# Kernel tuning notes

Hardware: AMD Instinct MI355X
Metric: run time of the kernel (lower is better)

Reference implementation:

```python
import jax, jax.numpy as jnp
import numpy as np

ALPHA, GAMMA = 0.25, 2.0
CLASS_W, COORD_W, MASK_W = 2.0, 5.0, 5.0
EPS = 1e-8


def point_sample(masks, coords):
    """Bilinear sample (grid_sample, align_corners=False, zero padding).
    masks: [R, H, W]; coords: [P, 2] as (x, y) in [0, 1]. Returns [R, P]."""
    H, W = masks.shape[-2:]
    gx = 2.0 * coords[:, 0] - 1.0
    gy = 2.0 * coords[:, 1] - 1.0
    x = ((gx + 1.0) * W - 1.0) * 0.5
    y = ((gy + 1.0) * H - 1.0) * 0.5
    x0 = jnp.floor(x)
    y0 = jnp.floor(y)
    wx1 = x - x0
    wy1 = y - y0
    wx0 = 1.0 - wx1
    wy0 = 1.0 - wy1
    x0i = x0.astype(jnp.int32)
    y0i = y0.astype(jnp.int32)
    x1i = x0i + 1
    y1i = y0i + 1

    def gather(ix, iy):
        valid = ((ix >= 0) & (ix < W) & (iy >= 0) & (iy < H)).astype(masks.dtype)
        ixc = jnp.clip(ix, 0, W - 1)
        iyc = jnp.clip(iy, 0, H - 1)
        return masks[:, iyc, ixc] * valid  # [R, P]

    return (gather(x0i, y0i) * (wx0 * wy0)
            + gather(x1i, y0i) * (wx1 * wy0)
            + gather(x0i, y1i) * (wx0 * wy1)
            + gather(x1i, y1i) * (wx1 * wy1))


def setup_inputs() -> dict:
    key = jax.random.key(0)
    k1, k2, k3, k4, k5, k6 = jax.random.split(key, 6)
    bs, Q, n_ctrl, Hm, Wm, T, P = 8, 300, 16, 128, 128, 160, 12544
    return {
        "pred_logits": jax.random.normal(k1, (bs, Q, 1), jnp.float32),
        "pred_ctrl_points": jax.random.uniform(k2, (bs, Q, n_ctrl, 2), jnp.float32),
        "pred_seg_mask": jax.random.normal(k3, (bs, Q, Hm, Wm), jnp.float32),
        "tgt_pts": jax.random.uniform(k4, (T, n_ctrl, 2), jnp.float32),
        "tgt_masks": jax.random.uniform(k5, (T, Hm, Wm), jnp.float32),
        "point_coords": jax.random.uniform(k6, (P, 2), jnp.float32),
        "lvl": 0,
    }


def reference(pred_logits, pred_ctrl_points, pred_seg_mask, tgt_pts, tgt_masks, point_coords, lvl):
    bs, Q = pred_logits.shape[:2]
    out_prob = jax.nn.sigmoid(pred_logits.reshape(bs * Q, -1))          # [N, 1]
    out_pts = pred_ctrl_points.reshape(bs * Q, -1)                      # [N, 2*n_ctrl]
    tgt_flat = tgt_pts.reshape(tgt_pts.shape[0], -1)                    # [T, 2*n_ctrl]

    cost_mask_dice = 0.0
    if lvl < 2:  # num_seg_layers
        out_masks = pred_seg_mask.reshape(bs * Q, *pred_seg_mask.shape[-2:])
        # nearest-interp of tgt_masks to out_masks size is identity (same size)
        t_pts_samp = point_sample(tgt_masks, point_coords)              # [T, P]
        o_pts_samp = point_sample(out_masks, point_coords)              # [N, P]
        s = jax.nn.sigmoid(o_pts_samp)                                  # dice_loss sigmoids inputs
        numerator = 2.0 * jnp.einsum('np,tp->nt', s, t_pts_samp)        # [N, T]
        denominator = s.sum(-1)[:, None] + t_pts_samp.sum(-1)[None, :]
        cost_mask_dice = 1.0 - (numerator + 1.0) / (denominator + 1.0)

    neg_cost = (1.0 - ALPHA) * out_prob ** GAMMA * (-jnp.log(1.0 - out_prob + EPS))
    pos_cost = ALPHA * (1.0 - out_prob) ** GAMMA * (-jnp.log(out_prob + EPS))
    cost_class = pos_cost - neg_cost                                    # [N, 1]

    cost_kpts = jnp.abs(out_pts[:, None, :] - tgt_flat[None, :, :]).sum(-1)  # L1 cdist [N, T]

    C = CLASS_W * cost_class + COORD_W * cost_kpts + MASK_W * cost_mask_dice
    return C.reshape(bs, Q, -1)
```

## Files before the change

### kernel.cpp

```cpp
#include <hip/hip_runtime.h>
#include <hip/hip_bf16.h>
#include <cstdint>

#define HW 128
#define MASK_ELEMS (HW * HW)
#define SBLK 1024
#define NBLK 256

typedef unsigned short ushort_t;
typedef __attribute__((ext_vector_type(4))) unsigned short ushort4_t;
typedef __attribute__((ext_vector_type(8))) short short8;
typedef __attribute__((ext_vector_type(4))) float f32x4;

__device__ __forceinline__ float asf(unsigned int u) {
    union { unsigned int i; float f; } c;
    c.i = u;
    return c.f;
}
__device__ __forceinline__ ushort_t f2bf(float f) {
    union { float f; unsigned int i; } c;
    c.f = f;
    unsigned int r = c.i + 0x7FFFu + ((c.i >> 16) & 1u);
    return (ushort_t)(r >> 16);
}

__global__ void kprep(const float* __restrict__ coords, int* __restrict__ idx,
                      uint2* __restrict__ wpk, int P) {
    int i = blockIdx.x * 256 + threadIdx.x;
    if (i >= P) return;
    float cx = coords[2 * i], cy = coords[2 * i + 1];
    float x = cx * (float)HW - 0.5f;
    float y = cy * (float)HW - 0.5f;
    float x0f = floorf(x), y0f = floorf(y);
    float wx1 = x - x0f, wy1 = y - y0f;
    float wx0 = 1.f - wx1, wy0 = 1.f - wy1;
    int x0 = (int)x0f, y0 = (int)y0f;

    float wxA = (x0 >= 0) ? wx0 : wx1;
    float wxB = (x0 >= 0 && x0 < HW - 1) ? wx1 : 0.f;
    float wyA = (y0 >= 0) ? wy0 : wy1;
    float wyB = (y0 >= 0 && y0 < HW - 1) ? wy1 : 0.f;
    int bx = max(x0, 0), by = max(y0, 0);
    if (bx > HW - 2) { bx = HW - 2; wxB = wxA; wxA = 0.f; }
    if (by > HW - 2) { by = HW - 2; wyB = wyA; wyA = 0.f; }

    idx[i] = by * HW + bx;
    wpk[i] = make_uint2((unsigned)f2bf(wxA * wyA) | ((unsigned)f2bf(wxB * wyA) << 16),
                        (unsigned)f2bf(wxA * wyB) | ((unsigned)f2bf(wxB * wyB) << 16));
}

__device__ __forceinline__ void stage_mask(const float* __restrict__ g, float* l, int tid) {
    #pragma unroll
    for (int j = 0; j < MASK_ELEMS / (SBLK * 4); ++j) {
        int o = j * SBLK * 4 + tid * 4;
        __builtin_amdgcn_global_load_lds(
            (const __attribute__((address_space(1))) unsigned int*)(const void*)(g + o),
            (__attribute__((address_space(3))) unsigned int*)(void*)(l + o), 16, 0, 0);
    }
}

__global__ __launch_bounds__(SBLK, 4) void ksamp_all(
        const float* __restrict__ pmask, const float* __restrict__ tmasks,
        const int* __restrict__ idx, const uint2* __restrict__ wpk,
        ushort_t* __restrict__ S, ushort_t* __restrict__ tsamp,
        float* __restrict__ ssum, float* __restrict__ tsum,
        const int* __restrict__ lvl, int N, int T, int P) {
    if (*lvl >= 2) return;
    __shared__ float buf[2][MASK_ELEMS];
    __shared__ float wred[2][SBLK / 64];
    int tid = threadIdx.x;
    int NM = N + T;
    int nq = P >> 2;

    int4 idr[4];
    uint4 war[4], wbr[4];
    #pragma unroll
    for (int it = 0; it < 4; ++it) {
        int q = it * SBLK + tid;
        if (q < nq) {
            idr[it] = ((const int4*)idx)[q];
            war[it] = ((const uint4*)wpk)[2 * q];
            wbr[it] = ((const uint4*)wpk)[2 * q + 1];
        } else {
            idr[it] = make_int4(0, 0, 0, 0);
            war[it] = make_uint4(0, 0, 0, 0);
            wbr[it] = make_uint4(0, 0, 0, 0);
        }
    }

    int b = blockIdx.x;
    if (b < NM) {
        const float* m0 = (b < N) ? pmask + (size_t)b * MASK_ELEMS
                                  : tmasks + (size_t)(b - N) * MASK_ELEMS;
        stage_mask(m0, buf[0], tid);
    }
    asm volatile("s_waitcnt vmcnt(0)" ::: "memory");
    __syncthreads();

    int cur = 0, cnt = 0;
    for (int mi = b; mi < NM; mi += NBLK, ++cnt) {
        int nxt = mi + NBLK;
        if (nxt < NM) {
            const float* mn = (nxt < N) ? pmask + (size_t)nxt * MASK_ELEMS
                                        : tmasks + (size_t)(nxt - N) * MASK_ELEMS;
            stage_mask(mn, buf[cur ^ 1], tid);
        }
        const float* lm = buf[cur];
        bool sig = (mi < N);
        ushort4_t* o4 = sig ? (ushort4_t*)(S + (size_t)mi * P)
                            : (ushort4_t*)(tsamp + (size_t)(mi - N) * P);
        float sum = 0.f;
        #pragma unroll
        for (int it = 0; it < 4; ++it) {
            int q = it * SBLK + tid;
            if (q < nq) {
                float v[4];
                int bi[4] = {idr[it].x, idr[it].y, idr[it].z, idr[it].w};
                unsigned wa[4] = {war[it].x, war[it].z, wbr[it].x, wbr[it].z};
                unsigned wb[4] = {war[it].y, war[it].w, wbr[it].y, wbr[it].w};
                #pragma unroll
                for (int p2 = 0; p2 < 4; ++p2) {
                    int bb = bi[p2];
                    float t00 = lm[bb], t01 = lm[bb + 1];
                    float t10 = lm[bb + HW], t11 = lm[bb + HW + 1];
                    float vv = asf(wa[p2] << 16) * t00 + asf(wa[p2] & 0xffff0000u) * t01
                             + asf(wb[p2] << 16) * t10 + asf(wb[p2] & 0xffff0000u) * t11;
                    if (sig) vv = __builtin_amdgcn_rcpf(1.f + __expf(-vv));
                    v[p2] = vv;
                }
                ushort4_t o = {f2bf(v[0]), f2bf(v[1]), f2bf(v[2]), f2bf(v[3])};
                o4[q] = o;
                sum += (v[0] + v[1]) + (v[2] + v[3]);
            }
        }
        #pragma unroll
        for (int m2 = 32; m2 > 0; m2 >>= 1) sum += __shfl_xor(sum, m2, 64);
        if ((tid & 63) == 0) wred[cnt & 1][tid >> 6] = sum;
        asm volatile("s_waitcnt vmcnt(0)" ::: "memory");
        __syncthreads();
        if (tid == 0) {
            float s = 0.f;
            #pragma unroll
            for (int w2 = 0; w2 < SBLK / 64; ++w2) s += wred[cnt & 1][w2];
            if (sig) ssum[mi] = s;
            else tsum[mi - N] = s;
        }
        cur ^= 1;
    }
}

#define LDF(Aarr, Barr, kof)                                                              \
    do {                                                                                  \
        _Pragma("unroll") for (int m_ = 0; m_ < 3; ++m_)                                  \
            Aarr[m_] = *(const short8*)(pa + (size_t)m_ * 16 * P + (kof));                \
        _Pragma("unroll") for (int j_ = 0; j_ < 5; ++j_)                                  \
            Barr[j_] = *(const short8*)(pb + (size_t)j_ * 16 * P + (kof));                \
    } while (0)

#define FMAS(Aarr, Barr)                                                                  \
    do {                                                                                  \
        _Pragma("unroll") for (int m_ = 0; m_ < 3; ++m_) {                                \
            _Pragma("unroll") for (int j_ = 0; j_ < 5; ++j_)                              \
                acc[m_][j_] = __builtin_amdgcn_mfma_f32_16x16x32_bf16(                    \
                    Aarr[m_], Barr[j_], acc[m_][j_], 0, 0, 0);                            \
        }                                                                                 \
    } while (0)

__global__ __launch_bounds__(256) void kgemm(const ushort_t* __restrict__ S,
                                             const ushort_t* __restrict__ Tm,
                                             float* __restrict__ Cpart,
                                             const int* __restrict__ lvl,
                                             int N, int T, int P, int nsteps) {
    if (*lvl >= 2) return;
    int tid = threadIdx.x;
    int wid = tid >> 6, lane = tid & 63;
    int wm = wid >> 1, wt = wid & 1;
    int r = lane & 15, g = lane >> 4;
    int n0 = blockIdx.x * 96 + wm * 48;
    int t0 = wt * 80;
    size_t k0 = (size_t)blockIdx.y * nsteps * 32 + g * 8;
    const ushort_t* pa = S + (size_t)(n0 + r) * P + k0;
    const ushort_t* pb = Tm + (size_t)(t0 + r) * P + k0;

    f32x4 acc[3][5];
    #pragma unroll
    for (int m2 = 0; m2 < 3; ++m2)
        #pragma unroll
        for (int j2 = 0; j2 < 5; ++j2) acc[m2][j2] = (f32x4){0.f, 0.f, 0.f, 0.f};

    short8 a0[3], b0[5], a1[3], b1[5];
    LDF(a0, b0, 0);
    int ks = 0;
    for (; ks + 2 < nsteps; ks += 2) {
        LDF(a1, b1, (ks + 1) * 32);
        FMAS(a0, b0);
        LDF(a0, b0, (ks + 2) * 32);
        FMAS(a1, b1);
    }
    LDF(a1, b1, (ks + 1) * 32);
    FMAS(a0, b0);
    FMAS(a1, b1);

    size_t cb = (size_t)blockIdx.y * N * T;
    #pragma unroll
    for (int m2 = 0; m2 < 3; ++m2)
        #pragma unroll
        for (int j2 = 0; j2 < 5; ++j2)
            #pragma unroll
            for (int q = 0; q < 4; ++q) {
                int row = n0 + m2 * 16 + g * 4 + q;
                int col = t0 + j2 * 16 + r;
                Cpart[cb + (size_t)row * T + col] = acc[m2][j2][q];
            }
}

__global__ void kfinal(const float* __restrict__ logits, const float* __restrict__ opts,
                       const float* __restrict__ tpts, const float* __restrict__ Cpart,
                       const float* __restrict__ ssum, const float* __restrict__ tsum,
                       const int* __restrict__ lvl, float* __restrict__ out,
                       int N, int T, int nks) {
    int idx = blockIdx.x * 256 + threadIdx.x;
    if (idx >= N * T) return;
    int n = idx / T, t = idx - n * T;

    float lg = logits[n];
    float p = 1.f / (1.f + __expf(-lg));
    float pos = 0.25f * (1.f - p) * (1.f - p) * (-logf(p + 1e-8f));
    float neg = 0.75f * p * p * (-logf(1.f - p + 1e-8f));
    float ccls = pos - neg;

    float kp = 0.f;
    const float4* a4 = (const float4*)(opts + (size_t)n * 32);
    const float4* b4 = (const float4*)(tpts + (size_t)t * 32);
    #pragma unroll
    for (int j = 0; j < 8; ++j) {
        float4 a = a4[j], b = b4[j];
        kp += fabsf(a.x - b.x) + fabsf(a.y - b.y) + fabsf(a.z - b.z) + fabsf(a.w - b.w);
    }

    float dice = 0.f;
    if (*lvl < 2) {
        float dot = 0.f;
        for (int ks = 0; ks < nks; ++ks) dot += Cpart[(size_t)ks * N * T + idx];
        dice = 1.f - (2.f * dot + 1.f) / (ssum[n] + tsum[t] + 1.f);
    }
    out[idx] = 2.f * ccls + 5.f * kp + 5.f * dice;
}

extern "C" void kernel_launch(void* const* d_in, const int* in_sizes, int n_in,
                              void* d_out, int out_size, void* d_ws, size_t ws_size,
                              hipStream_t stream) {
    const float* logits = (const float*)d_in[0];
    const float* cpts   = (const float*)d_in[1];
    const float* pmask  = (const float*)d_in[2];
    const float* tpts   = (const float*)d_in[3];
    const float* tmasks = (const float*)d_in[4];
    const float* coords = (const float*)d_in[5];
    const int*   lvl    = (const int*)d_in[6];
    float* out = (float*)d_out;

    int N = in_sizes[0];
    int T = in_sizes[3] / 32;
    int P = in_sizes[5] / 2;

    char* w = (char*)d_ws;
    auto alloc = [&](size_t bytes) {
        char* r = w;
        w += (bytes + 255) & ~(size_t)255;
        return r;
    };
    int*      idxb  = (int*)alloc((size_t)P * 4);
    uint2*    wpkb  = (uint2*)alloc((size_t)P * 8);
    ushort_t* tsamp = (ushort_t*)alloc((size_t)T * P * 2);
    ushort_t* S     = (ushort_t*)alloc((size_t)N * P * 2);
    float*    ssumb = (float*)alloc((size_t)N * 4);
    float*    tsumb = (float*)alloc((size_t)T * 4);
    size_t base_bytes = (size_t)(w - (char*)d_ws);

    int nks = 28;
    if (base_bytes + (size_t)nks * N * T * 4 > ws_size) nks = 14;
    if (base_bytes + (size_t)nks * N * T * 4 > ws_size) nks = 7;
    int nsteps = (P / 32) / nks;
    float* Cpart = (float*)alloc((size_t)nks * N * T * 4);

    kprep<<<(P + 255) / 256, 256, 0, stream>>>(coords, idxb, wpkb, P);
    ksamp_all<<<NBLK, SBLK, 0, stream>>>(pmask, tmasks, idxb, wpkb, S, tsamp,
                                         ssumb, tsumb, lvl, N, T, P);
    kgemm<<<dim3(N / 96, nks), 256, 0, stream>>>(S, tsamp, Cpart, lvl, N, T, P, nsteps);
    kfinal<<<(N * T + 255) / 256, 256, 0, stream>>>(logits, cpts, tpts, Cpart, ssumb, tsumb,
                                                    lvl, out, N, T, nks);
}
```

Measured before the change: 120.1 us.

## Shrink per-thread sample registers with LDS tail table and halve GEMM K-split

The sampling kernel keeps register-resident sample indices and weights for only three of the four point chunks. The small leftover tail of points (P/4 - 3072 = 64 quads) now sits in shared memory and is handled by one lane per 16 threads, which cuts register pressure. The launch-bounds occupancy hint is dropped and __syncthreads is replaced by explicit waitcnt plus s_barrier. The GEMM split-K count goes from 28 to 14, giving fewer partial buffers for the final kernel to reduce at the cost of fewer GEMM blocks.

```diff
diff --git a/kernel.cpp b/kernel.cpp
--- a/kernel.cpp
+++ b/kernel.cpp
@@ -59,7 +59,7 @@
     }
 }
 
-__global__ __launch_bounds__(SBLK, 4) void ksamp_all(
+__global__ __launch_bounds__(SBLK) void ksamp_all(
         const float* __restrict__ pmask, const float* __restrict__ tmasks,
         const int* __restrict__ idx, const uint2* __restrict__ wpk,
         ushort_t* __restrict__ S, ushort_t* __restrict__ tsamp,
@@ -68,14 +68,17 @@
     if (*lvl >= 2) return;
     __shared__ float buf[2][MASK_ELEMS];
     __shared__ float wred[2][SBLK / 64];
-    int tid = threadIdx.x;
-    int NM = N + T;
-    int nq = P >> 2;
-
-    int4 idr[4];
-    uint4 war[4], wbr[4];
-    #pragma unroll
-    for (int it = 0; it < 4; ++it) {
+    __shared__ int4  tmi[64];
+    __shared__ uint4 tma[64], tmb[64];
+    const int tid = threadIdx.x;
+    const int NM = N + T;
+    const int nq = P >> 2;
+    const int ntail = nq - 3 * SBLK;
+
+    int4 idr[3];
+    uint4 war[3], wbr[3];
+    #pragma unroll
+    for (int it = 0; it < 3; ++it) {
         int q = it * SBLK + tid;
         if (q < nq) {
             idr[it] = ((const int4*)idx)[q];
@@ -88,60 +91,83 @@
         }
     }
 
-    int b = blockIdx.x;
-    if (b < NM) {
-        const float* m0 = (b < N) ? pmask + (size_t)b * MASK_ELEMS
-                                  : tmasks + (size_t)(b - N) * MASK_ELEMS;
-        stage_mask(m0, buf[0], tid);
+    auto mptr = [&](int mi) -> const float* {
+        return (mi < N) ? pmask + (size_t)mi * MASK_ELEMS
+                        : tmasks + (size_t)(mi - N) * MASK_ELEMS;
+    };
+
+    const int b = blockIdx.x;
+    const int rounds = (NM - b + NBLK - 1) / NBLK;
+    if (rounds <= 0) return;
+
+    stage_mask(mptr(b), buf[0], tid);
+    if (ntail > 0 && ntail <= 64 && tid < ntail) {
+        int q = 3 * SBLK + tid;
+        tmi[tid] = ((const int4*)idx)[q];
+        tma[tid] = ((const uint4*)wpk)[2 * q];
+        tmb[tid] = ((const uint4*)wpk)[2 * q + 1];
     }
     asm volatile("s_waitcnt vmcnt(0)" ::: "memory");
-    __syncthreads();
-
-    int cur = 0, cnt = 0;
-    for (int mi = b; mi < NM; mi += NBLK, ++cnt) {
-        int nxt = mi + NBLK;
-        if (nxt < NM) {
-            const float* mn = (nxt < N) ? pmask + (size_t)nxt * MASK_ELEMS
-                                        : tmasks + (size_t)(nxt - N) * MASK_ELEMS;
-            stage_mask(mn, buf[cur ^ 1], tid);
-        }
+    asm volatile("s_waitcnt lgkmcnt(0)" ::: "memory");
+    __builtin_amdgcn_s_barrier();
+
+    int cur = 0;
+    for (int k = 0; k < rounds; ++k) {
+        if (k + 1 < rounds)
+            stage_mask(mptr(b + (k + 1) * NBLK), buf[cur ^ 1], tid);
+
         const float* lm = buf[cur];
-        bool sig = (mi < N);
+        const int mi = b + k * NBLK;
+        const bool sig = (mi < N);
         ushort4_t* o4 = sig ? (ushort4_t*)(S + (size_t)mi * P)
                             : (ushort4_t*)(tsamp + (size_t)(mi - N) * P);
         float sum = 0.f;
+
+        auto do_quad = [&](int4 id, uint4 wa4, uint4 wb4, int q) {
+            float v[4];
+            int bi[4] = {id.x, id.y, id.z, id.w};
+            unsigned wa[4] = {wa4.x, wa4.z, wb4.x, wb4.z};
+            unsigned wb[4] = {wa4.y, wa4.w, wb4.y, wb4.w};
+            #pragma unroll
+            for (int p2 = 0; p2 < 4; ++p2) {
+                int bb = bi[p2];
+                float t00 = lm[bb], t01 = lm[bb + 1];
+                float t10 = lm[bb + HW], t11 = lm[bb + HW + 1];
+                float vv = asf(wa[p2] << 16) * t00 + asf(wa[p2] & 0xffff0000u) * t01
+                         + asf(wb[p2] << 16) * t10 + asf(wb[p2] & 0xffff0000u) * t11;
+                if (sig) vv = __builtin_amdgcn_rcpf(1.f + __expf(-vv));
+                v[p2] = vv;
+            }
+            ushort4_t o = {f2bf(v[0]), f2bf(v[1]), f2bf(v[2]), f2bf(v[3])};
+            o4[q] = o;
+            sum += (v[0] + v[1]) + (v[2] + v[3]);
+        };
+
         #pragma unroll
-        for (int it = 0; it < 4; ++it) {
+        for (int it = 0; it < 3; ++it) {
             int q = it * SBLK + tid;
-            if (q < nq) {
-                float v[4];
-                int bi[4] = {idr[it].x, idr[it].y, idr[it].z, idr[it].w};
-                unsigned wa[4] = {war[it].x, war[it].z, wbr[it].x, wbr[it].z};
-                unsigned wb[4] = {war[it].y, war[it].w, wbr[it].y, wbr[it].w};
-                #pragma unroll
-                for (int p2 = 0; p2 < 4; ++p2) {
-                    int bb = bi[p2];
-                    float t00 = lm[bb], t01 = lm[bb + 1];
-                    float t10 = lm[bb + HW], t11 = lm[bb + HW + 1];
-                    float vv = asf(wa[p2] << 16) * t00 + asf(wa[p2] & 0xffff0000u) * t01
-                             + asf(wb[p2] << 16) * t10 + asf(wb[p2] & 0xffff0000u) * t11;
-                    if (sig) vv = __builtin_amdgcn_rcpf(1.f + __expf(-vv));
-                    v[p2] = vv;
-                }
-                ushort4_t o = {f2bf(v[0]), f2bf(v[1]), f2bf(v[2]), f2bf(v[3])};
-                o4[q] = o;
-                sum += (v[0] + v[1]) + (v[2] + v[3]);
-            }
+            if (q < nq) do_quad(idr[it], war[it], wbr[it], q);
         }
+        if (ntail > 0 && ntail <= 64) {
+            int tq = tid >> 4;
+            if (((tid & 15) == 0) && tq < ntail)
+                do_quad(tmi[tq], tma[tq], tmb[tq], 3 * SBLK + tq);
+        } else if (ntail > 64) {
+            for (int q = 3 * SBLK + tid; q < nq; q += SBLK)
+                do_quad(((const int4*)idx)[q], ((const uint4*)wpk)[2 * q],
+                        ((const uint4*)wpk)[2 * q + 1], q);
+        }
+
         #pragma unroll
         for (int m2 = 32; m2 > 0; m2 >>= 1) sum += __shfl_xor(sum, m2, 64);
-        if ((tid & 63) == 0) wred[cnt & 1][tid >> 6] = sum;
+        if ((tid & 63) == 0) wred[k & 1][tid >> 6] = sum;
         asm volatile("s_waitcnt vmcnt(0)" ::: "memory");
-        __syncthreads();
+        asm volatile("s_waitcnt lgkmcnt(0)" ::: "memory");
+        __builtin_amdgcn_s_barrier();
         if (tid == 0) {
             float s = 0.f;
             #pragma unroll
-            for (int w2 = 0; w2 < SBLK / 64; ++w2) s += wred[cnt & 1][w2];
+            for (int w2 = 0; w2 < SBLK / 64; ++w2) s += wred[k & 1][w2];
             if (sig) ssum[mi] = s;
             else tsum[mi - N] = s;
         }
@@ -277,8 +303,7 @@
     float*    tsumb = (float*)alloc((size_t)T * 4);
     size_t base_bytes = (size_t)(w - (char*)d_ws);
 
-    int nks = 28;
-    if (base_bytes + (size_t)nks * N * T * 4 > ws_size) nks = 14;
+    int nks = 14;
     if (base_bytes + (size_t)nks * N * T * 4 > ws_size) nks = 7;
     int nsteps = (P / 32) / nks;
     float* Cpart = (float*)alloc((size_t)nks * N * T * 4);
```

New measurement: 129.8 us. +8.1%, slower.
